# Performance work log

Hardware: AMD Instinct MI355X
Metric: run time of the kernel (lower is better)

## Reference

```python
import jax, jax.numpy as jnp
import numpy as np

IN_CH, OUT_CH, SUPPORT = 128, 128, 3
BS, N = 8, 2048


def knn_idx(x, k):
    # x: (bs, n, d) -> (bs, n, k) indices of k nearest (excluding self)
    sq = jnp.sum(x * x, axis=-1)  # (bs, n)
    dist = sq[:, :, None] + sq[:, None, :] - 2.0 * jnp.einsum('bnd,bmd->bnm', x, x)
    _, idx = jax.lax.top_k(-dist, k + 1)  # smallest distances
    return idx[:, :, 1:]


def gather_neighbors(t, idx):
    # t: (bs, n, d), idx: (bs, n, k) -> (bs, n, k, d)
    return jax.vmap(lambda tb, ib: tb[ib])(t, idx)


def l2_normalize(x, axis, eps=1e-12):
    n = jnp.linalg.norm(x, axis=axis, keepdims=True)
    return x / jnp.maximum(n, eps)


def setup_inputs() -> dict:
    key = jax.random.key(0)
    ks = jax.random.split(key, 8)
    stdv = 1.0 / np.sqrt(OUT_CH * (SUPPORT + 1))
    return {
        'vertices': jax.random.normal(ks[0], (BS, N, 3), jnp.float32),
        'feature_map': jax.random.normal(ks[1], (BS, N, IN_CH), jnp.float32),
        'weights': jax.random.uniform(ks[2], (IN_CH, (SUPPORT + 1) * OUT_CH), jnp.float32, -stdv, stdv),
        'bias': jax.random.uniform(ks[3], ((SUPPORT + 1) * OUT_CH,), jnp.float32, -stdv, stdv),
        'directions': jax.random.uniform(ks[4], (3, SUPPORT * OUT_CH), jnp.float32, -stdv, stdv),
        'ste_w': jax.random.normal(ks[5], (OUT_CH, IN_CH), jnp.float32) * (1.0 / np.sqrt(IN_CH)),
        'conv2_w': jax.random.normal(ks[6], (OUT_CH, 2 * OUT_CH), jnp.float32) * (1.0 / np.sqrt(2 * OUT_CH)),
        'neighbor_num': 16,
    }


def reference(vertices, feature_map, weights, bias, directions, ste_w, conv2_w, neighbor_num):
    bs, n, _ = vertices.shape
    k = neighbor_num

    # STE branch: 1x1 conv == per-point linear
    f_ste = jnp.einsum('bnc,oc->bno', feature_map, ste_w)

    # Receptive fields: KNN in feature space ('RF-F'), directions from vertices
    neighbor_index = knn_idx(feature_map, k)                      # (bs, n, k)
    neighbors = gather_neighbors(vertices, neighbor_index)        # (bs, n, k, 3)
    rf_norm = l2_normalize(neighbors - vertices[:, :, None, :], axis=-1)

    # Graph convolution (3D-GCN style)
    sdn = l2_normalize(directions, axis=0)                        # (3, s*out)
    theta = jax.nn.relu(jnp.einsum('bnkd,dm->bnkm', rf_norm, sdn))  # (bs,n,k,s*out)
    fm = feature_map @ weights + bias                             # (bs,n,(s+1)*out)
    feature_center = fm[:, :, :OUT_CH]
    feature_support = gather_neighbors(fm[:, :, OUT_CH:], neighbor_index)  # (bs,n,k,s*out)
    act = (theta * feature_support).reshape(bs, n, k, SUPPORT, OUT_CH)
    act = jnp.max(act, axis=2)          # max over neighbors
    act = jnp.mean(act, axis=2)         # mean over supports
    feature = feature_center + act      # (bs, n, out)

    # ORL: global context via point-space KNN max-pool
    nb_idx2 = knn_idx(vertices, k)
    pooled = jnp.max(gather_neighbors(feature, nb_idx2), axis=2)  # (bs,n,out)
    f_global = jnp.broadcast_to(jnp.mean(pooled, axis=1, keepdims=True), (bs, n, OUT_CH))
    feat_cat = jnp.concatenate([feature, f_global], axis=-1)      # (bs,n,2*out)
    feature_fuse = jnp.einsum('bnc,oc->bno', feat_cat, conv2_w) + feature

    return feature_fuse + f_ste
```

## Files before the change

### kernel.cpp

```cpp
#include <hip/hip_runtime.h>
#include <hip/hip_bf16.h>

#define BS 8
#define NP 2048
#define CIN 128
#define OC 128
#define NSUP 3
#define KNN 16
#define NC 512
#define SC 384
#define CAND 24

typedef __attribute__((ext_vector_type(8))) short bf16x8;
typedef __attribute__((ext_vector_type(4))) float f32x4;

__device__ inline unsigned short f2bf(float x) {
    __hip_bfloat16 h = __float2bfloat16(x);
    return *reinterpret_cast<unsigned short*>(&h);
}
__device__ inline float bf2f(short s) {
    unsigned u = ((unsigned)(unsigned short)s) << 16;
    return __uint_as_float(u);
}
__device__ inline unsigned fkey(float d, int gi) {
    unsigned u = __float_as_uint(d);
    u ^= (unsigned)((int)u >> 31) | 0x80000000u;
    return (u & 0xFFFFF800u) | (unsigned)gi;
}
__device__ inline unsigned umn(unsigned a, unsigned b) { return a < b ? a : b; }
__device__ inline unsigned umx(unsigned a, unsigned b) { return a > b ? a : b; }
__device__ inline void cswap(unsigned& a, unsigned& b) {
    unsigned t = umn(a, b); b = umx(a, b); a = t;
}
__device__ inline unsigned dpp_prev(unsigned v) {
    return (unsigned)__builtin_amdgcn_update_dpp(0, (int)v, 0x111, 0xF, 0xF, true);
}
__device__ inline unsigned third_smallest8(const unsigned kv[8]) {
    unsigned s0=kv[0],s1=kv[1],s2=kv[2],s3=kv[3],s4=kv[4],s5=kv[5],s6=kv[6],s7=kv[7];
    cswap(s0,s1); cswap(s2,s3); cswap(s4,s5); cswap(s6,s7);
    cswap(s0,s2); cswap(s1,s3); cswap(s4,s6); cswap(s5,s7);
    cswap(s1,s2); cswap(s5,s6); cswap(s0,s4); cswap(s3,s7);
    cswap(s1,s5); cswap(s2,s6);
    cswap(s1,s4); cswap(s3,s6);
    cswap(s2,s4); cswap(s3,s5);
    cswap(s3,s4);
    return s2;
}

__global__ __launch_bounds__(256) void prep_kernel(const float* __restrict__ in,
                                                   float* __restrict__ sq,
                                                   short* __restrict__ outp,
                                                   const float* __restrict__ W,
                                                   const float* __restrict__ conv2,
                                                   const float* __restrict__ stew,
                                                   const float* __restrict__ dirs,
                                                   short* __restrict__ Wt,
                                                   short* __restrict__ conv2b,
                                                   short* __restrict__ stewb,
                                                   float4* __restrict__ sdnn4) {
    const int tid = threadIdx.x;
    if (blockIdx.x < 1024) {
        const int row = blockIdx.x * 16 + (tid >> 4);
        const int seg = tid & 15;
        const float* p = in + (size_t)row * CIN + seg * 8;
        float4 f0 = *(const float4*)p;
        float4 f1 = *(const float4*)(p + 4);
        bf16x8 s;
        s[0] = (short)f2bf(f0.x); s[1] = (short)f2bf(f0.y);
        s[2] = (short)f2bf(f0.z); s[3] = (short)f2bf(f0.w);
        s[4] = (short)f2bf(f1.x); s[5] = (short)f2bf(f1.y);
        s[6] = (short)f2bf(f1.z); s[7] = (short)f2bf(f1.w);
        *(bf16x8*)&outp[(size_t)row * CIN + seg * 8] = s;
        float ss = f0.x*f0.x + f0.y*f0.y + f0.z*f0.z + f0.w*f0.w
                 + f1.x*f1.x + f1.y*f1.y + f1.z*f1.z + f1.w*f1.w;
#pragma unroll
        for (int msk = 1; msk <= 8; msk <<= 1) ss += __shfl_xor(ss, msk);
        if (seg == 0) sq[row] = ss;
    } else if (blockIdx.x < 1472) {
        int idx = (blockIdx.x - 1024) * 256 + tid;
        if (idx < NC * CIN) {
            int n = idx >> 7, k = idx & 127;
            Wt[idx] = (short)f2bf(W[(size_t)k * NC + n]);
        } else if (idx < NC * CIN + OC * 2 * OC) {
            int e = idx - NC * CIN;
            conv2b[e] = (short)f2bf(conv2[e]);
        } else {
            int e = idx - NC * CIN - OC * 2 * OC;
            stewb[e] = (short)f2bf(stew[e]);
        }
    } else {
        int m = (blockIdx.x - 1472) * 256 + tid;
        if (m < SC) {
            float d0 = dirs[m], d1 = dirs[SC + m], d2 = dirs[2 * SC + m];
            float nrm = sqrtf(d0 * d0 + d1 * d1 + d2 * d2);
            float den = fmaxf(nrm, 1e-12f);
            sdnn4[m] = make_float4(d0 / den, d1 / den, d2 / den, 0.f);
        }
    }
}

#define TQF 32
#define TPF 64
#define NCHF (NP / TPF)
__global__ __launch_bounds__(256) void knn_feat_kernel(const short* __restrict__ fbb,
                                                       const float* __restrict__ sqn,
                                                       int* __restrict__ cand) {
    __shared__ alignas(16) short Qb[TQF][128];
    __shared__ alignas(16) short Pb[TPF][128];
    __shared__ float sqP[TPF];
    __shared__ unsigned Ds[TQF][68];

    const int b = blockIdx.y, q0 = blockIdx.x * TQF, tid = threadIdx.x;
    const int lane = tid & 63, wid = tid >> 6;
    const short* fb = fbb + (size_t)b * NP * CIN;

    unsigned l0 = 0xFFFFFFFFu, l1 = 0xFFFFFFFFu, l2 = 0xFFFFFFFFu;
    unsigned T = 0xFFFFFFFFu;
    const int gbase = lane & 56;
    const int sub = lane & 7;

    for (int i = 0; i < 2; ++i) {
        int v = i * 256 + tid, row = v >> 4, g = v & 15;
        *(bf16x8*)&Qb[row][(g ^ (row & 7)) * 8] =
            *(const bf16x8*)&fb[(size_t)(q0 + row) * CIN + g * 8];
    }
    for (int i = 0; i < 4; ++i) {
        int v = i * 256 + tid, row = v >> 4, g = v & 15;
        *(bf16x8*)&Pb[row][(g ^ (row & 7)) * 8] =
            *(const bf16x8*)&fb[(size_t)row * CIN + g * 8];
    }
    if (tid < TPF) sqP[tid] = sqn[b * NP + tid];

    const int qt = wid >> 1, ph = wid & 1;
    const int qsl = tid >> 3;
    const int arow = qt * 16 + (lane & 15), asw = arow & 7;
    const int brow0 = ph * 32 + (lane & 15), brow1 = brow0 + 16;
    const int bsw0 = brow0 & 7, bsw1 = brow1 & 7;
    const int oct = lane >> 4;
    const int qrow = qt * 16 + oct * 4;

    for (int ch = 0; ch < NCHF; ++ch) {
        __syncthreads();
        bf16x8 st0, st1, st2, st3;
        float sq_next = 0.f;
        const int nxt = (ch + 1 < NCHF);
        if (nxt) {
            int p0n = (ch + 1) * TPF;
            { int v = tid;       int row = v>>4, g = v&15; st0 = *(const bf16x8*)&fb[(size_t)(p0n+row)*CIN + g*8]; }
            { int v = 256 + tid; int row = v>>4, g = v&15; st1 = *(const bf16x8*)&fb[(size_t)(p0n+row)*CIN + g*8]; }
            { int v = 512 + tid; int row = v>>4, g = v&15; st2 = *(const bf16x8*)&fb[(size_t)(p0n+row)*CIN + g*8]; }
            { int v = 768 + tid; int row = v>>4, g = v&15; st3 = *(const bf16x8*)&fb[(size_t)(p0n+row)*CIN + g*8]; }
            if (tid < TPF) sq_next = sqn[b * NP + p0n + tid];
        }
        f32x4 acc0 = {0.f,0.f,0.f,0.f}, acc1 = {0.f,0.f,0.f,0.f};
#pragma unroll
        for (int kk = 0; kk < 4; ++kk) {
            int g = kk * 4 + oct;
            bf16x8 av  = *(const bf16x8*)&Qb[arow][(g ^ asw) * 8];
            bf16x8 bv0 = *(const bf16x8*)&Pb[brow0][(g ^ bsw0) * 8];
            bf16x8 bv1 = *(const bf16x8*)&Pb[brow1][(g ^ bsw1) * 8];
            acc0 = __builtin_amdgcn_mfma_f32_16x16x32_bf16(av, bv0, acc0, 0, 0, 0);
            acc1 = __builtin_amdgcn_mfma_f32_16x16x32_bf16(av, bv1, acc1, 0, 0, 0);
        }
        const float sp0 = sqP[brow0], sp1 = sqP[brow1];
        const int pg0 = ch * TPF + brow0, pg1 = ch * TPF + brow1;
#pragma unroll
        for (int r = 0; r < 4; ++r) {
            int qg = q0 + qrow + r;
            unsigned k0 = fkey(sp0 - 2.0f * acc0[r], pg0);
            unsigned k1 = fkey(sp1 - 2.0f * acc1[r], pg1);
            if (qg == pg0) k0 = 0xFFFFFFFFu;
            if (qg == pg1) k1 = 0xFFFFFFFFu;
            Ds[qrow + r][brow0] = k0;
            Ds[qrow + r][brow1] = k1;
        }
        __syncthreads();

        {
            uint4 kA = *(const uint4*)&Ds[qsl][sub * 8];
            uint4 kB = *(const uint4*)&Ds[qsl][sub * 8 + 4];
            unsigned kv[8] = {kA.x, kA.y, kA.z, kA.w, kB.x, kB.y, kB.z, kB.w};
            if (ch == 0) {
                unsigned m3 = third_smallest8(kv);
                m3 = umx(m3, (unsigned)__shfl_xor((int)m3, 1));
                m3 = umx(m3, (unsigned)__shfl_xor((int)m3, 2));
                m3 = umx(m3, (unsigned)__shfl_xor((int)m3, 4));
                T = m3 + 1;
            }
#pragma unroll
            for (int j = 0; j < 8; ++j) {
                unsigned long long bal = __ballot(kv[j] < T);
                unsigned gm = (unsigned)(bal >> gbase) & 0xFFu;
                while (gm) {
                    int l = __builtin_ctz(gm);
                    gm &= gm - 1;
                    unsigned k = (unsigned)__shfl((int)kv[j], gbase + l);
                    unsigned pv = dpp_prev(l2);
                    if (sub == 0) pv = 0u;
                    unsigned n0 = umn(umx(pv, k), l0);
                    unsigned n1 = umn(umx(l0, k), l1);
                    unsigned n2 = umn(umx(l1, k), l2);
                    l0 = n0; l1 = n1; l2 = n2;
                }
            }
            T = (unsigned)__shfl((int)l2, gbase + 7);
        }
        if (nxt) {
            { int v = tid;       int row = v>>4, g = v&15; *(bf16x8*)&Pb[row][(g^(row&7))*8] = st0; }
            { int v = 256 + tid; int row = v>>4, g = v&15; *(bf16x8*)&Pb[row][(g^(row&7))*8] = st1; }
            { int v = 512 + tid; int row = v>>4, g = v&15; *(bf16x8*)&Pb[row][(g^(row&7))*8] = st2; }
            { int v = 768 + tid; int row = v>>4, g = v&15; *(bf16x8*)&Pb[row][(g^(row&7))*8] = st3; }
            if (tid < TPF) sqP[tid] = sq_next;
        }
    }

    {
        int* dst = cand + ((size_t)b * NP + q0 + qsl) * CAND;
        dst[3 * sub + 0] = (int)(l0 & 0x7FFu);
        dst[3 * sub + 1] = (int)(l1 & 0x7FFu);
        dst[3 * sub + 2] = (int)(l2 & 0x7FFu);
    }
}

__global__ __launch_bounds__(256) void knn_refine_kernel(const float* __restrict__ feat,
                                                         const int* __restrict__ cand,
                                                         int* __restrict__ nbr) {
    __shared__ unsigned long long keyS[4][CAND];
    const int w = threadIdx.x >> 6;
    const int lane = threadIdx.x & 63;
    const int grp = lane >> 4, sl = lane & 15;
    const int gq = blockIdx.x * 4 + w;
    const int b = gq >> 11;
    const int q = gq & (NP - 1);
    const float* fb = feat + (size_t)b * NP * CIN;

    double qd[8];
    {
        float4 a = *(const float4*)&fb[(size_t)q * CIN + sl * 8];
        float4 c = *(const float4*)&fb[(size_t)q * CIN + sl * 8 + 4];
        qd[0] = a.x; qd[1] = a.y; qd[2] = a.z; qd[3] = a.w;
        qd[4] = c.x; qd[5] = c.y; qd[6] = c.z; qd[7] = c.w;
    }
    double sqd = 0.0;
#pragma unroll
    for (int i = 0; i < 8; ++i) sqd += qd[i] * qd[i];
#pragma unroll
    for (int msk = 1; msk <= 8; msk <<= 1) sqd += __shfl_xor(sqd, msk);
    const float sqi = (float)sqd;

    const int* cq = cand + (size_t)gq * CAND;
    int jv[CAND / 4];
#pragma unroll
    for (int t = 0; t < CAND / 4; ++t) jv[t] = cq[t * 4 + grp];

#pragma unroll
    for (int t = 0; t < CAND / 4; ++t) {
        const int j = jv[t];
        float4 a = *(const float4*)&fb[(size_t)j * CIN + sl * 8];
        float4 c = *(const float4*)&fb[(size_t)j * CIN + sl * 8 + 4];
        double fd[8] = {a.x, a.y, a.z, a.w, c.x, c.y, c.z, c.w};
        double dot = 0.0, sj = 0.0;
#pragma unroll
        for (int i = 0; i < 8; ++i) { dot += qd[i] * fd[i]; sj += fd[i] * fd[i]; }
#pragma unroll
        for (int msk = 1; msk <= 8; msk <<= 1) {
            dot += __shfl_xor(dot, msk);
            sj  += __shfl_xor(sj, msk);
        }
        if (sl == 0) {
            float t1 = sqi + (float)sj;
            float t2 = (float)(2.0 * dot);
            float d32 = t1 - t2;
            unsigned u = __float_as_uint(d32);
            u ^= (unsigned)((int)u >> 31) | 0x80000000u;
            keyS[w][t * 4 + grp] = ((unsigned long long)u << 32) | (unsigned)j;
        }
    }
    __syncthreads();
    if (lane < CAND) {
        unsigned long long k = keyS[w][lane];
        int rank = 0;
#pragma unroll
        for (int m = 0; m < CAND; ++m) rank += (keyS[w][m] < k) ? 1 : 0;
        if (rank < KNN) nbr[(size_t)gq * KNN + rank] = (int)(k & 0xFFFFFFFFu);
    }
}

#define TQV 32
__global__ __launch_bounds__(256) void knn_vert_kernel(const float* __restrict__ vert,
                                                       int* __restrict__ nbr) {
    __shared__ alignas(16) float vx[NP], vy[NP], vz[NP];
    const int b = blockIdx.y;
    const int q0 = blockIdx.x * TQV;
    const int tid = threadIdx.x;
    const float* vb = vert + (size_t)b * NP * 3;

    for (int i = 0; i < NP * 3 / 256; ++i) {
        int e = i * 256 + tid;
        float v = vb[e];
        int row = e / 3, comp = e % 3;
        (comp == 0 ? vx : comp == 1 ? vy : vz)[row] = v;
    }
    __syncthreads();

    const int lane = tid & 63;
    const int gbase = lane & 56;
    const int q = tid >> 3;
    const int sub = tid & 7;
    const float qx = vx[q0 + q], qy = vy[q0 + q], qz = vz[q0 + q];

    unsigned l0 = 0xFFFFFFFFu, l1 = 0xFFFFFFFFu, l2 = 0xFFFFFFFFu;
    unsigned T = 0xFFFFFFFFu;

    for (int m = 0; m < NP / 64; ++m) {
        const int p0 = m * 64 + sub * 8;
        float4 xA = *(const float4*)&vx[p0], xB = *(const float4*)&vx[p0 + 4];
        float4 yA = *(const float4*)&vy[p0], yB = *(const float4*)&vy[p0 + 4];
        float4 zA = *(const float4*)&vz[p0], zB = *(const float4*)&vz[p0 + 4];
        float dv[8];
        { float dx = qx-xA.x, dy = qy-yA.x, dz = qz-zA.x; dv[0] = dx*dx+dy*dy+dz*dz; }
        { float dx = qx-xA.y, dy = qy-yA.y, dz = qz-zA.y; dv[1] = dx*dx+dy*dy+dz*dz; }
        { float dx = qx-xA.z, dy = qy-yA.z, dz = qz-zA.z; dv[2] = dx*dx+dy*dy+dz*dz; }
        { float dx = qx-xA.w, dy = qy-yA.w, dz = qz-zA.w; dv[3] = dx*dx+dy*dy+dz*dz; }
        { float dx = qx-xB.x, dy = qy-yB.x, dz = qz-zB.x; dv[4] = dx*dx+dy*dy+dz*dz; }
        { float dx = qx-xB.y, dy = qy-yB.y, dz = qz-zB.y; dv[5] = dx*dx+dy*dy+dz*dz; }
        { float dx = qx-xB.z, dy = qy-yB.z, dz = qz-zB.z; dv[6] = dx*dx+dy*dy+dz*dz; }
        { float dx = qx-xB.w, dy = qy-yB.w, dz = qz-zB.w; dv[7] = dx*dx+dy*dy+dz*dz; }
        unsigned kv[8];
#pragma unroll
        for (int j = 0; j < 8; ++j) kv[j] = fkey(dv[j], p0 + j);
        if (m == 0) {
            unsigned m3 = third_smallest8(kv);
            m3 = umx(m3, (unsigned)__shfl_xor((int)m3, 1));
            m3 = umx(m3, (unsigned)__shfl_xor((int)m3, 2));
            m3 = umx(m3, (unsigned)__shfl_xor((int)m3, 4));
            T = m3 + 1;
        }
#pragma unroll
        for (int j = 0; j < 8; ++j) {
            unsigned long long bal = __ballot(kv[j] < T);
            unsigned gm = (unsigned)(bal >> gbase) & 0xFFu;
            while (gm) {
                int l = __builtin_ctz(gm);
                gm &= gm - 1;
                unsigned k = (unsigned)__shfl((int)kv[j], gbase + l);
                unsigned pv = dpp_prev(l2);
                if (sub == 0) pv = 0u;
                unsigned n0 = umn(umx(pv, k), l0);
                unsigned n1 = umn(umx(l0, k), l1);
                unsigned n2 = umn(umx(l1, k), l2);
                l0 = n0; l1 = n1; l2 = n2;
            }
        }
        T = (unsigned)__shfl((int)l2, gbase + 7);
    }
    {
        int* dst = nbr + ((size_t)b * NP + q0 + q) * KNN;
        unsigned vals[3] = {l0, l1, l2};
#pragma unroll
        for (int e = 0; e < 3; ++e) {
            int r = 3 * sub + e;
            if (r >= 1 && r <= 16) dst[r - 1] = (int)(vals[e] & 0x7FFu);
        }
    }
}

__global__ __launch_bounds__(256) void fm_gemm_kernel(const short* __restrict__ fbb,
                                                      const short* __restrict__ Wt,
                                                      const float* __restrict__ bias,
                                                      float* __restrict__ centerf,
                                                      short* __restrict__ supb) {
    __shared__ alignas(16) short As[64][128];
    const int m0 = blockIdx.x * 64, n0 = blockIdx.y * 128, tid = threadIdx.x;
    const int lane = tid & 63, wid = tid >> 6, oct = lane >> 4;
    for (int i = 0; i < 4; ++i) {
        int v = i * 256 + tid, row = v >> 4, g = v & 15;
        *(bf16x8*)&As[row][(g ^ (row & 7)) * 8] =
            *(const bf16x8*)&fbb[(size_t)(m0 + row) * CIN + g * 8];
    }
    __syncthreads();
    f32x4 acc[4][2] = {};
#pragma unroll
    for (int kk = 0; kk < 4; ++kk) {
        int g = kk * 4 + oct;
        bf16x8 bv[2];
#pragma unroll
        for (int nt = 0; nt < 2; ++nt) {
            int n = n0 + (wid * 2 + nt) * 16 + (lane & 15);
            bv[nt] = *(const bf16x8*)&Wt[(size_t)n * CIN + g * 8];
        }
#pragma unroll
        for (int mt = 0; mt < 4; ++mt) {
            int ar = mt * 16 + (lane & 15);
            bf16x8 av = *(const bf16x8*)&As[ar][(g ^ (ar & 7)) * 8];
#pragma unroll
            for (int nt = 0; nt < 2; ++nt)
                acc[mt][nt] = __builtin_amdgcn_mfma_f32_16x16x32_bf16(av, bv[nt], acc[mt][nt], 0, 0, 0);
        }
    }
#pragma unroll
    for (int mt = 0; mt < 4; ++mt)
#pragma unroll
        for (int nt = 0; nt < 2; ++nt) {
            int n = n0 + (wid * 2 + nt) * 16 + (lane & 15);
            float bsv = bias[n];
            int mbase = m0 + mt * 16 + oct * 4;
#pragma unroll
            for (int r = 0; r < 4; ++r) {
                float val = acc[mt][nt][r] + bsv;
                if (n0 == 0)
                    centerf[(size_t)(mbase + r) * OC + n] = val;
                else
                    supb[(size_t)(mbase + r) * SC + (n - OC)] = (short)f2bf(val);
            }
        }
}

__global__ __launch_bounds__(128) void act_kernel(const float* __restrict__ centerf,
                                                  const short* __restrict__ supb,
                                                  const int* __restrict__ nbr,
                                                  const float* __restrict__ vert,
                                                  const float4* __restrict__ sdnn4,
                                                  float* __restrict__ feature,
                                                  short* __restrict__ featb) {
    __shared__ int sj[KNN];
    __shared__ float rf[KNN][4];
    const int i = blockIdx.x;
    const int b = blockIdx.y;
    const int tid = threadIdx.x;
    const size_t bi = (size_t)b * NP + i;
    if (tid < KNN) {
        int j = nbr[bi * KNN + tid];
        sj[tid] = j;
        const float* vb = vert + (size_t)b * NP * 3;
        float dx = vb[j * 3 + 0] - vb[i * 3 + 0];
        float dy = vb[j * 3 + 1] - vb[i * 3 + 1];
        float dz = vb[j * 3 + 2] - vb[i * 3 + 2];
        float nrm = sqrtf(dx * dx + dy * dy + dz * dz);
        float den = fmaxf(nrm, 1e-12f);
        rf[tid][0] = dx / den; rf[tid][1] = dy / den; rf[tid][2] = dz / den;
    }
    __syncthreads();
    const int oc = tid;
    float accm = 0.0f;
#pragma unroll
    for (int s = 0; s < NSUP; ++s) {
        int m = s * OC + oc;
        float4 sv = sdnn4[m];
        float s0 = sv.x, s1 = sv.y, s2 = sv.z;
        float vm[4] = {-3.0e38f, -3.0e38f, -3.0e38f, -3.0e38f};
#pragma unroll
        for (int kk = 0; kk < KNN; ++kk) {
            float th = fmaxf(rf[kk][0] * s0 + rf[kk][1] * s1 + rf[kk][2] * s2, 0.0f);
            float sup = bf2f(supb[((size_t)b * NP + sj[kk]) * SC + m]);
            vm[kk & 3] = fmaxf(vm[kk & 3], th * sup);
        }
        accm += fmaxf(fmaxf(vm[0], vm[1]), fmaxf(vm[2], vm[3]));
    }
    float v = centerf[bi * OC + oc] + accm / 3.0f;
    feature[bi * OC + oc] = v;
    featb[bi * OC + oc] = (short)f2bf(v);
}

__global__ __launch_bounds__(128) void pool_kernel(const short* __restrict__ featb,
                                                   const int* __restrict__ nbr2,
                                                   float* __restrict__ pooled) {
    __shared__ int sj[KNN];
    const int i = blockIdx.x, b = blockIdx.y, tid = threadIdx.x;
    const size_t bi = (size_t)b * NP + i;
    if (tid < KNN) sj[tid] = nbr2[bi * KNN + tid];
    __syncthreads();
    float m0 = -3.0e38f, m1 = -3.0e38f, m2 = -3.0e38f, m3 = -3.0e38f;
#pragma unroll
    for (int kk = 0; kk < KNN; kk += 4) {
        m0 = fmaxf(m0, bf2f(featb[((size_t)b * NP + sj[kk + 0]) * OC + tid]));
        m1 = fmaxf(m1, bf2f(featb[((size_t)b * NP + sj[kk + 1]) * OC + tid]));
        m2 = fmaxf(m2, bf2f(featb[((size_t)b * NP + sj[kk + 2]) * OC + tid]));
        m3 = fmaxf(m3, bf2f(featb[((size_t)b * NP + sj[kk + 3]) * OC + tid]));
    }
    pooled[bi * OC + tid] = fmaxf(fmaxf(m0, m1), fmaxf(m2, m3));
}

__global__ __launch_bounds__(128) void partial_kernel(const float* __restrict__ pooled,
                                                      float* __restrict__ part) {
    const int ch = blockIdx.x, b = blockIdx.y, tid = threadIdx.x;
    float s0 = 0.f, s1 = 0.f, s2 = 0.f, s3 = 0.f;
    const float* base = pooled + ((size_t)b * NP + ch * 128) * OC + tid;
    for (int i = 0; i < 128; i += 4) {
        s0 += base[(size_t)(i + 0) * OC];
        s1 += base[(size_t)(i + 1) * OC];
        s2 += base[(size_t)(i + 2) * OC];
        s3 += base[(size_t)(i + 3) * OC];
    }
    part[((size_t)b * 16 + ch) * OC + tid] = ((s0 + s1) + (s2 + s3));
}
__global__ __launch_bounds__(128) void fg_gdot_kernel(const float* __restrict__ part,
                                                      const float* __restrict__ conv2,
                                                      float* __restrict__ gd) {
    __shared__ float fgs[OC];
    const int b = blockIdx.x, tid = threadIdx.x;
    float s = 0.f;
#pragma unroll
    for (int c = 0; c < 16; ++c) s += part[((size_t)b * 16 + c) * OC + tid];
    fgs[tid] = s / (float)NP;
    __syncthreads();
    float g = 0.f;
    const float* w = conv2 + (size_t)tid * 2 * OC + OC;
    for (int c = 0; c < OC; ++c) g += fgs[c] * w[c];
    gd[b * OC + tid] = g;
}

__global__ __launch_bounds__(256) void final_kernel(const short* __restrict__ featb,
                                                    const short* __restrict__ fbb,
                                                    const short* __restrict__ conv2b,
                                                    const short* __restrict__ stewb,
                                                    const float* __restrict__ gd,
                                                    const float* __restrict__ feature,
                                                    float* __restrict__ out) {
    __shared__ alignas(16) short Af[32][128];
    __shared__ alignas(16) short Am[32][128];
    const int m0 = blockIdx.x * 32, tid = threadIdx.x;
    const int lane = tid & 63, wid = tid >> 6, oct = lane >> 4;
    for (int i = 0; i < 2; ++i) {
        int v = i * 256 + tid, row = v >> 4, g = v & 15;
        *(bf16x8*)&Af[row][(g ^ (row & 7)) * 8] =
            *(const bf16x8*)&featb[(size_t)(m0 + row) * OC + g * 8];
        *(bf16x8*)&Am[row][(g ^ (row & 7)) * 8] =
            *(const bf16x8*)&fbb[(size_t)(m0 + row) * CIN + g * 8];
    }
    __syncthreads();
    f32x4 acc[2][2] = {};
#pragma unroll
    for (int kk = 0; kk < 4; ++kk) {
        int g = kk * 4 + oct;
        bf16x8 bC[2], bS[2];
#pragma unroll
        for (int nt = 0; nt < 2; ++nt) {
            int n = (wid * 2 + nt) * 16 + (lane & 15);
            bC[nt] = *(const bf16x8*)&conv2b[(size_t)n * (2 * OC) + g * 8];
            bS[nt] = *(const bf16x8*)&stewb[(size_t)n * CIN + g * 8];
        }
#pragma unroll
        for (int mt = 0; mt < 2; ++mt) {
            int ar = mt * 16 + (lane & 15);
            bf16x8 aF = *(const bf16x8*)&Af[ar][(g ^ (ar & 7)) * 8];
            bf16x8 aM = *(const bf16x8*)&Am[ar][(g ^ (ar & 7)) * 8];
#pragma unroll
            for (int nt = 0; nt < 2; ++nt) {
                acc[mt][nt] = __builtin_amdgcn_mfma_f32_16x16x32_bf16(aF, bC[nt], acc[mt][nt], 0, 0, 0);
                acc[mt][nt] = __builtin_amdgcn_mfma_f32_16x16x32_bf16(aM, bS[nt], acc[mt][nt], 0, 0, 0);
            }
        }
    }
#pragma unroll
    for (int mt = 0; mt < 2; ++mt)
#pragma unroll
        for (int nt = 0; nt < 2; ++nt) {
            int o = (wid * 2 + nt) * 16 + (lane & 15);
            int mbase = m0 + mt * 16 + oct * 4;
#pragma unroll
            for (int r = 0; r < 4; ++r) {
                int m = mbase + r;
                out[(size_t)m * OC + o] = acc[mt][nt][r]
                    + gd[(m >> 11) * OC + o] + feature[(size_t)m * OC + o];
            }
        }
}

extern "C" void kernel_launch(void* const* d_in, const int* in_sizes, int n_in,
                              void* d_out, int out_size, void* d_ws, size_t ws_size,
                              hipStream_t stream) {
    const float* vert  = (const float*)d_in[0];
    const float* fmap  = (const float*)d_in[1];
    const float* W     = (const float*)d_in[2];
    const float* bias  = (const float*)d_in[3];
    const float* dirs  = (const float*)d_in[4];
    const float* stew  = (const float*)d_in[5];
    const float* conv2 = (const float*)d_in[6];
    float* out = (float*)d_out;

    float* ws      = (float*)d_ws;
    float* sqn     = ws;
    short* fbb     = (short*)(sqn + 16384);
    float* centerf = sqn + 16384 + 1048576;
    short* supb    = (short*)(centerf + 2097152);
    float* feature = centerf + 2097152 + 3145728;
    short* featb   = (short*)(feature + 2097152);
    float* gd      = feature + 2097152 + 1048576;
    short* Wt      = (short*)(gd + 1024);
    short* conv2b  = Wt + 65536;
    short* stewb   = conv2b + 32768;
    int*   nbr1    = (int*)(stewb + 16384);
    int*   nbr2    = nbr1 + 262144;
    float* part    = (float*)(nbr2 + 262144);
    float4* sdnn4  = (float4*)(part + 16384);
    int*   cand    = (int*)(sdnn4 + 384);
    float* pooled  = (float*)(cand + 393216);

    prep_kernel<<<1474, 256, 0, stream>>>(fmap, sqn, fbb, W, conv2, stew, dirs,
                                          Wt, conv2b, stewb, sdnn4);
    knn_feat_kernel<<<dim3(64, 8), 256, 0, stream>>>(fbb, sqn, cand);
    knn_refine_kernel<<<4096, 256, 0, stream>>>(fmap, cand, nbr1);
    knn_vert_kernel<<<dim3(64, 8), 256, 0, stream>>>(vert, nbr2);
    fm_gemm_kernel<<<dim3(256, 4), 256, 0, stream>>>(fbb, Wt, bias, centerf, supb);
    act_kernel<<<dim3(2048, 8), 128, 0, stream>>>(centerf, supb, nbr1, vert, sdnn4,
                                                  feature, featb);
    pool_kernel<<<dim3(2048, 8), 128, 0, stream>>>(featb, nbr2, pooled);
    partial_kernel<<<dim3(16, 8), 128, 0, stream>>>(pooled, part);
    fg_gdot_kernel<<<8, 128, 0, stream>>>(part, conv2, gd);
    final_kernel<<<512, 256, 0, stream>>>(featb, fbb, conv2b, stewb, gd, feature, out);
}
```

Before: 220.9 us.

## Merge feature-KNN, vertex-KNN and feature GEMM into one heterogeneous launch

```diff
diff --git a/kernel.cpp b/kernel.cpp
--- a/kernel.cpp
+++ b/kernel.cpp
@@ -102,85 +102,176 @@
 #define TQF 32
 #define TPF 64
 #define NCHF (NP / TPF)
-__global__ __launch_bounds__(256) void knn_feat_kernel(const short* __restrict__ fbb,
-                                                       const float* __restrict__ sqn,
-                                                       int* __restrict__ cand) {
-    __shared__ alignas(16) short Qb[TQF][128];
-    __shared__ alignas(16) short Pb[TPF][128];
-    __shared__ float sqP[TPF];
-    __shared__ unsigned Ds[TQF][68];
-
-    const int b = blockIdx.y, q0 = blockIdx.x * TQF, tid = threadIdx.x;
+#define SMEM_BYTES 33536
+__global__ __launch_bounds__(256) void fused_kernel(const short* __restrict__ fbb,
+                                                    const float* __restrict__ sqn,
+                                                    int* __restrict__ cand,
+                                                    const float* __restrict__ vert,
+                                                    int* __restrict__ nbr2,
+                                                    const short* __restrict__ Wt,
+                                                    const float* __restrict__ bias,
+                                                    float* __restrict__ centerf,
+                                                    short* __restrict__ supb) {
+    __shared__ alignas(16) unsigned char smem[SMEM_BYTES];
+    const int bx = blockIdx.x;
+    const int tid = threadIdx.x;
     const int lane = tid & 63, wid = tid >> 6;
-    const short* fb = fbb + (size_t)b * NP * CIN;
-
-    unsigned l0 = 0xFFFFFFFFu, l1 = 0xFFFFFFFFu, l2 = 0xFFFFFFFFu;
-    unsigned T = 0xFFFFFFFFu;
-    const int gbase = lane & 56;
-    const int sub = lane & 7;
-
-    for (int i = 0; i < 2; ++i) {
-        int v = i * 256 + tid, row = v >> 4, g = v & 15;
-        *(bf16x8*)&Qb[row][(g ^ (row & 7)) * 8] =
-            *(const bf16x8*)&fb[(size_t)(q0 + row) * CIN + g * 8];
-    }
-    for (int i = 0; i < 4; ++i) {
-        int v = i * 256 + tid, row = v >> 4, g = v & 15;
-        *(bf16x8*)&Pb[row][(g ^ (row & 7)) * 8] =
-            *(const bf16x8*)&fb[(size_t)row * CIN + g * 8];
-    }
-    if (tid < TPF) sqP[tid] = sqn[b * NP + tid];
-
-    const int qt = wid >> 1, ph = wid & 1;
-    const int qsl = tid >> 3;
-    const int arow = qt * 16 + (lane & 15), asw = arow & 7;
-    const int brow0 = ph * 32 + (lane & 15), brow1 = brow0 + 16;
-    const int bsw0 = brow0 & 7, bsw1 = brow1 & 7;
-    const int oct = lane >> 4;
-    const int qrow = qt * 16 + oct * 4;
-
-    for (int ch = 0; ch < NCHF; ++ch) {
+
+    if (bx < 512) {
+        short (*Qb)[128]   = (short (*)[128])smem;
+        short (*Pb)[128]   = (short (*)[128])(smem + 8192);
+        float* sqP         = (float*)(smem + 24576);
+        unsigned (*Ds)[68] = (unsigned (*)[68])(smem + 24832);
+
+        const int b = bx >> 6, q0 = (bx & 63) * TQF;
+        const short* fb = fbb + (size_t)b * NP * CIN;
+
+        unsigned l0 = 0xFFFFFFFFu, l1 = 0xFFFFFFFFu, l2 = 0xFFFFFFFFu;
+        unsigned T = 0xFFFFFFFFu;
+        const int gbase = lane & 56;
+        const int sub = lane & 7;
+
+        for (int i = 0; i < 2; ++i) {
+            int v = i * 256 + tid, row = v >> 4, g = v & 15;
+            *(bf16x8*)&Qb[row][(g ^ (row & 7)) * 8] =
+                *(const bf16x8*)&fb[(size_t)(q0 + row) * CIN + g * 8];
+        }
+        for (int i = 0; i < 4; ++i) {
+            int v = i * 256 + tid, row = v >> 4, g = v & 15;
+            *(bf16x8*)&Pb[row][(g ^ (row & 7)) * 8] =
+                *(const bf16x8*)&fb[(size_t)row * CIN + g * 8];
+        }
+        if (tid < TPF) sqP[tid] = sqn[b * NP + tid];
+
+        const int qt = wid >> 1, ph = wid & 1;
+        const int qsl = tid >> 3;
+        const int arow = qt * 16 + (lane & 15), asw = arow & 7;
+        const int brow0 = ph * 32 + (lane & 15), brow1 = brow0 + 16;
+        const int bsw0 = brow0 & 7, bsw1 = brow1 & 7;
+        const int oct = lane >> 4;
+        const int qrow = qt * 16 + oct * 4;
+
+        for (int ch = 0; ch < NCHF; ++ch) {
+            __syncthreads();
+            bf16x8 st0, st1, st2, st3;
+            float sq_next = 0.f;
+            const int nxt = (ch + 1 < NCHF);
+            if (nxt) {
+                int p0n = (ch + 1) * TPF;
+                { int v = tid;       int row = v>>4, g = v&15; st0 = *(const bf16x8*)&fb[(size_t)(p0n+row)*CIN + g*8]; }
+                { int v = 256 + tid; int row = v>>4, g = v&15; st1 = *(const bf16x8*)&fb[(size_t)(p0n+row)*CIN + g*8]; }
+                { int v = 512 + tid; int row = v>>4, g = v&15; st2 = *(const bf16x8*)&fb[(size_t)(p0n+row)*CIN + g*8]; }
+                { int v = 768 + tid; int row = v>>4, g = v&15; st3 = *(const bf16x8*)&fb[(size_t)(p0n+row)*CIN + g*8]; }
+                if (tid < TPF) sq_next = sqn[b * NP + p0n + tid];
+            }
+            f32x4 acc0 = {0.f,0.f,0.f,0.f}, acc1 = {0.f,0.f,0.f,0.f};
+#pragma unroll
+            for (int kk = 0; kk < 4; ++kk) {
+                int g = kk * 4 + oct;
+                bf16x8 av  = *(const bf16x8*)&Qb[arow][(g ^ asw) * 8];
+                bf16x8 bv0 = *(const bf16x8*)&Pb[brow0][(g ^ bsw0) * 8];
+                bf16x8 bv1 = *(const bf16x8*)&Pb[brow1][(g ^ bsw1) * 8];
+                acc0 = __builtin_amdgcn_mfma_f32_16x16x32_bf16(av, bv0, acc0, 0, 0, 0);
+                acc1 = __builtin_amdgcn_mfma_f32_16x16x32_bf16(av, bv1, acc1, 0, 0, 0);
+            }
+            const float sp0 = sqP[brow0], sp1 = sqP[brow1];
+            const int pg0 = ch * TPF + brow0, pg1 = ch * TPF + brow1;
+#pragma unroll
+            for (int r = 0; r < 4; ++r) {
+                int qg = q0 + qrow + r;
+                unsigned k0 = fkey(sp0 - 2.0f * acc0[r], pg0);
+                unsigned k1 = fkey(sp1 - 2.0f * acc1[r], pg1);
+                if (qg == pg0) k0 = 0xFFFFFFFFu;
+                if (qg == pg1) k1 = 0xFFFFFFFFu;
+                Ds[qrow + r][brow0] = k0;
+                Ds[qrow + r][brow1] = k1;
+            }
+            __syncthreads();
+            {
+                uint4 kA = *(const uint4*)&Ds[qsl][sub * 8];
+                uint4 kB = *(const uint4*)&Ds[qsl][sub * 8 + 4];
+                unsigned kv[8] = {kA.x, kA.y, kA.z, kA.w, kB.x, kB.y, kB.z, kB.w};
+                if (ch == 0) {
+                    unsigned m3 = third_smallest8(kv);
+                    m3 = umx(m3, (unsigned)__shfl_xor((int)m3, 1));
+                    m3 = umx(m3, (unsigned)__shfl_xor((int)m3, 2));
+                    m3 = umx(m3, (unsigned)__shfl_xor((int)m3, 4));
+                    T = m3 + 1;
+                }
+#pragma unroll
+                for (int j = 0; j < 8; ++j) {
+                    unsigned long long bal = __ballot(kv[j] < T);
+                    unsigned gm = (unsigned)(bal >> gbase) & 0xFFu;
+                    while (gm) {
+                        int l = __builtin_ctz(gm);
+                        gm &= gm - 1;
+                        unsigned k = (unsigned)__shfl((int)kv[j], gbase + l);
+                        unsigned pv = dpp_prev(l2);
+                        if (sub == 0) pv = 0u;
+                        unsigned n0 = umn(umx(pv, k), l0);
+                        unsigned n1 = umn(umx(l0, k), l1);
+                        unsigned n2 = umn(umx(l1, k), l2);
+                        l0 = n0; l1 = n1; l2 = n2;
+                    }
+                }
+                T = (unsigned)__shfl((int)l2, gbase + 7);
+            }
+            if (nxt) {
+                { int v = tid;       int row = v>>4, g = v&15; *(bf16x8*)&Pb[row][(g^(row&7))*8] = st0; }
+                { int v = 256 + tid; int row = v>>4, g = v&15; *(bf16x8*)&Pb[row][(g^(row&7))*8] = st1; }
+                { int v = 512 + tid; int row = v>>4, g = v&15; *(bf16x8*)&Pb[row][(g^(row&7))*8] = st2; }
+                { int v = 768 + tid; int row = v>>4, g = v&15; *(bf16x8*)&Pb[row][(g^(row&7))*8] = st3; }
+                if (tid < TPF) sqP[tid] = sq_next;
+            }
+        }
+        {
+            int* dst = cand + ((size_t)b * NP + q0 + qsl) * CAND;
+            dst[3 * sub + 0] = (int)(l0 & 0x7FFu);
+            dst[3 * sub + 1] = (int)(l1 & 0x7FFu);
+            dst[3 * sub + 2] = (int)(l2 & 0x7FFu);
+        }
+    } else if (bx < 1024) {
+        float* vx = (float*)smem;
+        float* vy = (float*)(smem + 8192);
+        float* vz = (float*)(smem + 16384);
+        const int bb = bx - 512;
+        const int b = bb >> 6, q0 = (bb & 63) * 32;
+        const float* vb = vert + (size_t)b * NP * 3;
+
+        for (int i = 0; i < NP * 3 / 256; ++i) {
+            int e = i * 256 + tid;
+            float v = vb[e];
+            int row = e / 3, comp = e % 3;
+            (comp == 0 ? vx : comp == 1 ? vy : vz)[row] = v;
+        }
         __syncthreads();
-        bf16x8 st0, st1, st2, st3;
-        float sq_next = 0.f;
-        const int nxt = (ch + 1 < NCHF);
-        if (nxt) {
-            int p0n = (ch + 1) * TPF;
-            { int v = tid;       int row = v>>4, g = v&15; st0 = *(const bf16x8*)&fb[(size_t)(p0n+row)*CIN + g*8]; }
-            { int v = 256 + tid; int row = v>>4, g = v&15; st1 = *(const bf16x8*)&fb[(size_t)(p0n+row)*CIN + g*8]; }
-            { int v = 512 + tid; int row = v>>4, g = v&15; st2 = *(const bf16x8*)&fb[(size_t)(p0n+row)*CIN + g*8]; }
-            { int v = 768 + tid; int row = v>>4, g = v&15; st3 = *(const bf16x8*)&fb[(size_t)(p0n+row)*CIN + g*8]; }
-            if (tid < TPF) sq_next = sqn[b * NP + p0n + tid];
-        }
-        f32x4 acc0 = {0.f,0.f,0.f,0.f}, acc1 = {0.f,0.f,0.f,0.f};
-#pragma unroll
-        for (int kk = 0; kk < 4; ++kk) {
-            int g = kk * 4 + oct;
-            bf16x8 av  = *(const bf16x8*)&Qb[arow][(g ^ asw) * 8];
-            bf16x8 bv0 = *(const bf16x8*)&Pb[brow0][(g ^ bsw0) * 8];
-            bf16x8 bv1 = *(const bf16x8*)&Pb[brow1][(g ^ bsw1) * 8];
-            acc0 = __builtin_amdgcn_mfma_f32_16x16x32_bf16(av, bv0, acc0, 0, 0, 0);
-            acc1 = __builtin_amdgcn_mfma_f32_16x16x32_bf16(av, bv1, acc1, 0, 0, 0);
-        }
-        const float sp0 = sqP[brow0], sp1 = sqP[brow1];
-        const int pg0 = ch * TPF + brow0, pg1 = ch * TPF + brow1;
-#pragma unroll
-        for (int r = 0; r < 4; ++r) {
-            int qg = q0 + qrow + r;
-            unsigned k0 = fkey(sp0 - 2.0f * acc0[r], pg0);
-            unsigned k1 = fkey(sp1 - 2.0f * acc1[r], pg1);
-            if (qg == pg0) k0 = 0xFFFFFFFFu;
-            if (qg == pg1) k1 = 0xFFFFFFFFu;
-            Ds[qrow + r][brow0] = k0;
-            Ds[qrow + r][brow1] = k1;
-        }
-        __syncthreads();
-
-        {
-            uint4 kA = *(const uint4*)&Ds[qsl][sub * 8];
-            uint4 kB = *(const uint4*)&Ds[qsl][sub * 8 + 4];
-            unsigned kv[8] = {kA.x, kA.y, kA.z, kA.w, kB.x, kB.y, kB.z, kB.w};
-            if (ch == 0) {
+
+        const int gbase = lane & 56;
+        const int q = tid >> 3;
+        const int sub = tid & 7;
+        const float qx = vx[q0 + q], qy = vy[q0 + q], qz = vz[q0 + q];
+
+        unsigned l0 = 0xFFFFFFFFu, l1 = 0xFFFFFFFFu, l2 = 0xFFFFFFFFu;
+        unsigned T = 0xFFFFFFFFu;
+
+        for (int m = 0; m < NP / 64; ++m) {
+            const int p0 = m * 64 + sub * 8;
+            float4 xA = *(const float4*)&vx[p0], xB = *(const float4*)&vx[p0 + 4];
+            float4 yA = *(const float4*)&vy[p0], yB = *(const float4*)&vy[p0 + 4];
+            float4 zA = *(const float4*)&vz[p0], zB = *(const float4*)&vz[p0 + 4];
+            float dv[8];
+            { float dx = qx-xA.x, dy = qy-yA.x, dz = qz-zA.x; dv[0] = dx*dx+dy*dy+dz*dz; }
+            { float dx = qx-xA.y, dy = qy-yA.y, dz = qz-zA.y; dv[1] = dx*dx+dy*dy+dz*dz; }
+            { float dx = qx-xA.z, dy = qy-yA.z, dz = qz-zA.z; dv[2] = dx*dx+dy*dy+dz*dz; }
+            { float dx = qx-xA.w, dy = qy-yA.w, dz = qz-zA.w; dv[3] = dx*dx+dy*dy+dz*dz; }
+            { float dx = qx-xB.x, dy = qy-yB.x, dz = qz-zB.x; dv[4] = dx*dx+dy*dy+dz*dz; }
+            { float dx = qx-xB.y, dy = qy-yB.y, dz = qz-zB.y; dv[5] = dx*dx+dy*dy+dz*dz; }
+            { float dx = qx-xB.z, dy = qy-yB.z, dz = qz-zB.z; dv[6] = dx*dx+dy*dy+dz*dz; }
+            { float dx = qx-xB.w, dy = qy-yB.w, dz = qz-zB.w; dv[7] = dx*dx+dy*dy+dz*dz; }
+            unsigned kv[8];
+#pragma unroll
+            for (int j = 0; j < 8; ++j) kv[j] = fkey(dv[j], p0 + j);
+            if (m == 0) {
                 unsigned m3 = third_smallest8(kv);
                 m3 = umx(m3, (unsigned)__shfl_xor((int)m3, 1));
                 m3 = umx(m3, (unsigned)__shfl_xor((int)m3, 2));
@@ -205,20 +296,61 @@
             }
             T = (unsigned)__shfl((int)l2, gbase + 7);
         }
-        if (nxt) {
-            { int v = tid;       int row = v>>4, g = v&15; *(bf16x8*)&Pb[row][(g^(row&7))*8] = st0; }
-            { int v = 256 + tid; int row = v>>4, g = v&15; *(bf16x8*)&Pb[row][(g^(row&7))*8] = st1; }
-            { int v = 512 + tid; int row = v>>4, g = v&15; *(bf16x8*)&Pb[row][(g^(row&7))*8] = st2; }
-            { int v = 768 + tid; int row = v>>4, g = v&15; *(bf16x8*)&Pb[row][(g^(row&7))*8] = st3; }
-            if (tid < TPF) sqP[tid] = sq_next;
-        }
-    }
-
-    {
-        int* dst = cand + ((size_t)b * NP + q0 + qsl) * CAND;
-        dst[3 * sub + 0] = (int)(l0 & 0x7FFu);
-        dst[3 * sub + 1] = (int)(l1 & 0x7FFu);
-        dst[3 * sub + 2] = (int)(l2 & 0x7FFu);
+        {
+            int* dst = nbr2 + ((size_t)b * NP + q0 + q) * KNN;
+            unsigned vals[3] = {l0, l1, l2};
+#pragma unroll
+            for (int e = 0; e < 3; ++e) {
+                int r = 3 * sub + e;
+                if (r >= 1 && r <= 16) dst[r - 1] = (int)(vals[e] & 0x7FFu);
+            }
+        }
+    } else {
+        short (*As)[128] = (short (*)[128])smem;
+        const int bb = bx - 1024;
+        const int m0 = (bb & 255) * 64, n0 = (bb >> 8) * 128;
+        const int oct = lane >> 4;
+        for (int i = 0; i < 4; ++i) {
+            int v = i * 256 + tid, row = v >> 4, g = v & 15;
+            *(bf16x8*)&As[row][(g ^ (row & 7)) * 8] =
+                *(const bf16x8*)&fbb[(size_t)(m0 + row) * CIN + g * 8];
+        }
+        __syncthreads();
+        f32x4 acc[4][2] = {};
+#pragma unroll
+        for (int kk = 0; kk < 4; ++kk) {
+            int g = kk * 4 + oct;
+            bf16x8 bv[2];
+#pragma unroll
+            for (int nt = 0; nt < 2; ++nt) {
+                int n = n0 + (wid * 2 + nt) * 16 + (lane & 15);
+                bv[nt] = *(const bf16x8*)&Wt[(size_t)n * CIN + g * 8];
+            }
+#pragma unroll
+            for (int mt = 0; mt < 4; ++mt) {
+                int ar = mt * 16 + (lane & 15);
+                bf16x8 av = *(const bf16x8*)&As[ar][(g ^ (ar & 7)) * 8];
+#pragma unroll
+                for (int nt = 0; nt < 2; ++nt)
+                    acc[mt][nt] = __builtin_amdgcn_mfma_f32_16x16x32_bf16(av, bv[nt], acc[mt][nt], 0, 0, 0);
+            }
+        }
+#pragma unroll
+        for (int mt = 0; mt < 4; ++mt)
+#pragma unroll
+            for (int nt = 0; nt < 2; ++nt) {
+                int n = n0 + (wid * 2 + nt) * 16 + (lane & 15);
+                float bsv = bias[n];
+                int mbase = m0 + mt * 16 + oct * 4;
+#pragma unroll
+                for (int r = 0; r < 4; ++r) {
+                    float val = acc[mt][nt][r] + bsv;
+                    if (n0 == 0)
+                        centerf[(size_t)(mbase + r) * OC + n] = val;
+                    else
+                        supb[(size_t)(mbase + r) * SC + (n - OC)] = (short)f2bf(val);
+                }
+            }
     }
 }
 
@@ -284,136 +416,6 @@
         for (int m = 0; m < CAND; ++m) rank += (keyS[w][m] < k) ? 1 : 0;
         if (rank < KNN) nbr[(size_t)gq * KNN + rank] = (int)(k & 0xFFFFFFFFu);
     }
-}
-
-#define TQV 32
-__global__ __launch_bounds__(256) void knn_vert_kernel(const float* __restrict__ vert,
-                                                       int* __restrict__ nbr) {
-    __shared__ alignas(16) float vx[NP], vy[NP], vz[NP];
-    const int b = blockIdx.y;
-    const int q0 = blockIdx.x * TQV;
-    const int tid = threadIdx.x;
-    const float* vb = vert + (size_t)b * NP * 3;
-
-    for (int i = 0; i < NP * 3 / 256; ++i) {
-        int e = i * 256 + tid;
-        float v = vb[e];
-        int row = e / 3, comp = e % 3;
-        (comp == 0 ? vx : comp == 1 ? vy : vz)[row] = v;
-    }
-    __syncthreads();
-
-    const int lane = tid & 63;
-    const int gbase = lane & 56;
-    const int q = tid >> 3;
-    const int sub = tid & 7;
-    const float qx = vx[q0 + q], qy = vy[q0 + q], qz = vz[q0 + q];
-
-    unsigned l0 = 0xFFFFFFFFu, l1 = 0xFFFFFFFFu, l2 = 0xFFFFFFFFu;
-    unsigned T = 0xFFFFFFFFu;
-
-    for (int m = 0; m < NP / 64; ++m) {
-        const int p0 = m * 64 + sub * 8;
-        float4 xA = *(const float4*)&vx[p0], xB = *(const float4*)&vx[p0 + 4];
-        float4 yA = *(const float4*)&vy[p0], yB = *(const float4*)&vy[p0 + 4];
-        float4 zA = *(const float4*)&vz[p0], zB = *(const float4*)&vz[p0 + 4];
-        float dv[8];
-        { float dx = qx-xA.x, dy = qy-yA.x, dz = qz-zA.x; dv[0] = dx*dx+dy*dy+dz*dz; }
-        { float dx = qx-xA.y, dy = qy-yA.y, dz = qz-zA.y; dv[1] = dx*dx+dy*dy+dz*dz; }
-        { float dx = qx-xA.z, dy = qy-yA.z, dz = qz-zA.z; dv[2] = dx*dx+dy*dy+dz*dz; }
-        { float dx = qx-xA.w, dy = qy-yA.w, dz = qz-zA.w; dv[3] = dx*dx+dy*dy+dz*dz; }
-        { float dx = qx-xB.x, dy = qy-yB.x, dz = qz-zB.x; dv[4] = dx*dx+dy*dy+dz*dz; }
-        { float dx = qx-xB.y, dy = qy-yB.y, dz = qz-zB.y; dv[5] = dx*dx+dy*dy+dz*dz; }
-        { float dx = qx-xB.z, dy = qy-yB.z, dz = qz-zB.z; dv[6] = dx*dx+dy*dy+dz*dz; }
-        { float dx = qx-xB.w, dy = qy-yB.w, dz = qz-zB.w; dv[7] = dx*dx+dy*dy+dz*dz; }
-        unsigned kv[8];
-#pragma unroll
-        for (int j = 0; j < 8; ++j) kv[j] = fkey(dv[j], p0 + j);
-        if (m == 0) {
-            unsigned m3 = third_smallest8(kv);
-            m3 = umx(m3, (unsigned)__shfl_xor((int)m3, 1));
-            m3 = umx(m3, (unsigned)__shfl_xor((int)m3, 2));
-            m3 = umx(m3, (unsigned)__shfl_xor((int)m3, 4));
-            T = m3 + 1;
-        }
-#pragma unroll
-        for (int j = 0; j < 8; ++j) {
-            unsigned long long bal = __ballot(kv[j] < T);
-            unsigned gm = (unsigned)(bal >> gbase) & 0xFFu;
-            while (gm) {
-                int l = __builtin_ctz(gm);
-                gm &= gm - 1;
-                unsigned k = (unsigned)__shfl((int)kv[j], gbase + l);
-                unsigned pv = dpp_prev(l2);
-                if (sub == 0) pv = 0u;
-                unsigned n0 = umn(umx(pv, k), l0);
-                unsigned n1 = umn(umx(l0, k), l1);
-                unsigned n2 = umn(umx(l1, k), l2);
-                l0 = n0; l1 = n1; l2 = n2;
-            }
-        }
-        T = (unsigned)__shfl((int)l2, gbase + 7);
-    }
-    {
-        int* dst = nbr + ((size_t)b * NP + q0 + q) * KNN;
-        unsigned vals[3] = {l0, l1, l2};
-#pragma unroll
-        for (int e = 0; e < 3; ++e) {
-            int r = 3 * sub + e;
-            if (r >= 1 && r <= 16) dst[r - 1] = (int)(vals[e] & 0x7FFu);
-        }
-    }
-}
-
-__global__ __launch_bounds__(256) void fm_gemm_kernel(const short* __restrict__ fbb,
-                                                      const short* __restrict__ Wt,
-                                                      const float* __restrict__ bias,
-                                                      float* __restrict__ centerf,
-                                                      short* __restrict__ supb) {
-    __shared__ alignas(16) short As[64][128];
-    const int m0 = blockIdx.x * 64, n0 = blockIdx.y * 128, tid = threadIdx.x;
-    const int lane = tid & 63, wid = tid >> 6, oct = lane >> 4;
-    for (int i = 0; i < 4; ++i) {
-        int v = i * 256 + tid, row = v >> 4, g = v & 15;
-        *(bf16x8*)&As[row][(g ^ (row & 7)) * 8] =
-            *(const bf16x8*)&fbb[(size_t)(m0 + row) * CIN + g * 8];
-    }
-    __syncthreads();
-    f32x4 acc[4][2] = {};
-#pragma unroll
-    for (int kk = 0; kk < 4; ++kk) {
-        int g = kk * 4 + oct;
-        bf16x8 bv[2];
-#pragma unroll
-        for (int nt = 0; nt < 2; ++nt) {
-            int n = n0 + (wid * 2 + nt) * 16 + (lane & 15);
-            bv[nt] = *(const bf16x8*)&Wt[(size_t)n * CIN + g * 8];
-        }
-#pragma unroll
-        for (int mt = 0; mt < 4; ++mt) {
-            int ar = mt * 16 + (lane & 15);
-            bf16x8 av = *(const bf16x8*)&As[ar][(g ^ (ar & 7)) * 8];
-#pragma unroll
-            for (int nt = 0; nt < 2; ++nt)
-                acc[mt][nt] = __builtin_amdgcn_mfma_f32_16x16x32_bf16(av, bv[nt], acc[mt][nt], 0, 0, 0);
-        }
-    }
-#pragma unroll
-    for (int mt = 0; mt < 4; ++mt)
-#pragma unroll
-        for (int nt = 0; nt < 2; ++nt) {
-            int n = n0 + (wid * 2 + nt) * 16 + (lane & 15);
-            float bsv = bias[n];
-            int mbase = m0 + mt * 16 + oct * 4;
-#pragma unroll
-            for (int r = 0; r < 4; ++r) {
-                float val = acc[mt][nt][r] + bsv;
-                if (n0 == 0)
-                    centerf[(size_t)(mbase + r) * OC + n] = val;
-                else
-                    supb[(size_t)(mbase + r) * SC + (n - OC)] = (short)f2bf(val);
-            }
-        }
 }
 
 __global__ __launch_bounds__(128) void act_kernel(const float* __restrict__ centerf,
@@ -599,10 +601,9 @@
 
     prep_kernel<<<1474, 256, 0, stream>>>(fmap, sqn, fbb, W, conv2, stew, dirs,
                                           Wt, conv2b, stewb, sdnn4);
-    knn_feat_kernel<<<dim3(64, 8), 256, 0, stream>>>(fbb, sqn, cand);
+    fused_kernel<<<2048, 256, 0, stream>>>(fbb, sqn, cand, vert, nbr2,
+                                           Wt, bias, centerf, supb);
     knn_refine_kernel<<<4096, 256, 0, stream>>>(fmap, cand, nbr1);
-    knn_vert_kernel<<<dim3(64, 8), 256, 0, stream>>>(vert, nbr2);
-    fm_gemm_kernel<<<dim3(256, 4), 256, 0, stream>>>(fbb, Wt, bias, centerf, supb);
     act_kernel<<<dim3(2048, 8), 128, 0, stream>>>(centerf, supb, nbr1, vert, sdnn4,
                                                   feature, featb);
     pool_kernel<<<dim3(2048, 8), 128, 0, stream>>>(featb, nbr2, pooled);
```

After: 205.9 us, median of 2. 1.07x faster.
